# Performance work log

Measured on AMD Instinct MI355X. Metric: run time of the kernel, lower is better.

## Reference

```python
import jax, jax.numpy as jnp
import numpy as np

DIM = 768
HEADS = 12
HEAD_DIM = DIM // HEADS
SCALE = HEAD_DIM ** (-0.5)
BATCH = 1
SEQ = 4096


def setup_inputs() -> dict:
    key = jax.random.key(0)
    ks = jax.random.split(key, 5)
    x = jax.random.normal(ks[0], (BATCH, SEQ, DIM), dtype=jnp.float32)
    # Linear params stored (in, out) for y = x @ W + b
    w_qkv = jax.random.normal(ks[1], (DIM, 3 * DIM), dtype=jnp.float32) * (DIM ** -0.5)
    b_qkv = jnp.zeros((3 * DIM,), dtype=jnp.float32)
    w_proj = jax.random.normal(ks[2], (DIM, DIM), dtype=jnp.float32) * (DIM ** -0.5)
    b_proj = jnp.zeros((DIM,), dtype=jnp.float32)
    return {"x": x, "w_qkv": w_qkv, "b_qkv": b_qkv, "w_proj": w_proj, "b_proj": b_proj}


def reference(x, w_qkv, b_qkv, w_proj, b_proj):
    B, S, _ = x.shape
    qkv = x @ w_qkv + b_qkv                              # [B,S,3*DIM]
    qkv = qkv.reshape(B, S, 3, HEADS, HEAD_DIM)
    q, k, v = qkv[:, :, 0], qkv[:, :, 1], qkv[:, :, 2]   # [B,S,H,D]
    # scaled dot-product attention, full score matrix as in the original
    attn = jnp.einsum("bqhd,bkhd->bhqk", q * SCALE, k)   # [B,H,S,S]
    attn = jax.nn.softmax(attn, axis=-1)
    out = jnp.einsum("bhqk,bkhd->bqhd", attn, v)         # [B,S,H,D]
    out = out.reshape(B, S, DIM)
    return out @ w_proj + b_proj
```

## Files before the change

kernel.cpp:

```cpp
#include <hip/hip_runtime.h>
#include <hip/hip_bf16.h>

#define SEQ   4096
#define DIM   768
#define HEADS 12
#define NQKV  2304
#define QSCALE 0.18033688011f

#if __has_builtin(__builtin_amdgcn_exp2f)
#define EXP2(x) __builtin_amdgcn_exp2f(x)
#else
#define EXP2(x) __expf((x) * 0.69314718056f)
#endif

typedef __bf16 bf16_t;
typedef bf16_t bf16x8 __attribute__((ext_vector_type(8)));
typedef float  f32x4  __attribute__((ext_vector_type(4)));
typedef float  f32x16 __attribute__((ext_vector_type(16)));
typedef unsigned short u16;
typedef unsigned int   u32;

static __device__ __forceinline__ float bf2f(u16 v) {
    union { float f; unsigned u; } x; x.u = ((unsigned)v) << 16; return x.f;
}
static __device__ __forceinline__ u16 f2bf(float f) {
    union { float f; unsigned u; } x; x.f = f;
    unsigned r = x.u + 0x7fff + ((x.u >> 16) & 1);
    return (u16)(r >> 16);
}
static __device__ __forceinline__ u32 fbits(float f) {
    union { float f; unsigned u; } x; x.f = f; return x.u;
}
static __device__ __forceinline__ void gload_lds16(const u16* g, u16* l) {
    __builtin_amdgcn_global_load_lds(
        (const __attribute__((address_space(1))) unsigned int*)g,
        (__attribute__((address_space(3))) unsigned int*)l, 16, 0, 0);
}

static __device__ __forceinline__ int detect_f32(const u32* __restrict__ x) {
    int lane = threadIdx.x & 63;
    int cnt = 0;
#pragma unroll
    for (int i = 0; i < 8; ++i) {
        u32 w = x[lane * 8 + i];
        cnt += (((w >> 7) & 0xFF) >= 0x8F) ? 1 : 0;
    }
#pragma unroll
    for (int m = 1; m < 64; m <<= 1) cnt += __shfl_xor(cnt, m);
    return cnt >= 64;
}

__global__ __launch_bounds__(256) void prep(
    const void* __restrict__ x, const void* __restrict__ wqkv,
    const void* __restrict__ bqkv, const void* __restrict__ wproj,
    const void* __restrict__ bproj,
    u16* __restrict__ cvt, u16* __restrict__ wqkvT, u16* __restrict__ wprojT)
{
    __shared__ u16 tile[64][65];
    const bool f32 = detect_f32((const u32*)x) != 0;
    const int b = blockIdx.x;
    const int t = threadIdx.x;

    if (b < 576) {
        const void* src; u16* dst; int K, N, tx, ty;
        if (b < 432) { src = wqkv; dst = wqkvT; K = DIM; N = NQKV; tx = b % 36; ty = b / 36; }
        else { int bb = b - 432; src = wproj; dst = wprojT; K = DIM; N = DIM; tx = bb % 12; ty = bb / 12; }
        const int k0 = ty * 64, n0 = tx * 64;
#pragma unroll
        for (int i = 0; i < 16; ++i) {
            int idx = i * 256 + t;
            int r = idx >> 6, c = idx & 63;
            size_t si = (size_t)(k0 + r) * N + n0 + c;
            tile[r][c] = f32 ? f2bf(((const float*)src)[si]) : ((const u16*)src)[si];
        }
        __syncthreads();
#pragma unroll
        for (int i = 0; i < 16; ++i) {
            int idx = i * 256 + t;
            int r = idx >> 6, c = idx & 63;
            dst[(size_t)(n0 + r) * K + k0 + c] = tile[c][r];
        }
    } else {
        const int SX = SEQ * DIM, e1 = SX + NQKV;
        const int n_cvt = e1 + DIM;
        for (int i = (b - 576) * 256 + t; i < n_cvt; i += 200 * 256) {
            const void* s; int off;
            if      (i < SX) { s = x; off = i; }
            else if (i < e1) { s = bqkv; off = i - SX; }
            else             { s = bproj; off = i - e1; }
            cvt[i] = f32 ? f2bf(((const float*)s)[off]) : ((const u16*)s)[off];
        }
    }
}

template<int MODE>
__global__ __launch_bounds__(256) void gemm128(
    const u16* __restrict__ A, const u16* __restrict__ BT, const u16* __restrict__ bias,
    u16* __restrict__ C0, float* __restrict__ Cf, u16* __restrict__ VT,
    const u32* __restrict__ xdet, int M, int N, int K)
{
    __shared__ u16 a_lds[128 * 32];
    __shared__ u16 b_lds[128 * 32];

    const int t    = threadIdx.x;
    const int w    = t >> 6;
    const int lane = t & 63;
    const int l15  = lane & 15;
    const int quad = lane >> 4;
    const int wm   = w >> 1, wn = w & 1;
    const int m0   = blockIdx.y * 128, n0 = blockIdx.x * 128;

    const int srow = w * 32 + (lane >> 2);
    const int kch  = (lane & 3) * 8;
    const u16* asrc = A  + (size_t)(m0 + srow) * K + kch;
    const u16* bsrc = BT + (size_t)(n0 + srow) * K + kch;
    u16* adst = a_lds + w * 32 * 32;
    u16* bdst = b_lds + w * 32 * 32;

    f32x4 acc[4][4] = {};

    for (int kt = 0; kt < K; kt += 32) {
        __syncthreads();
        gload_lds16(asrc,          adst);
        gload_lds16(asrc + 16 * K, adst + 16 * 32);
        gload_lds16(bsrc,          bdst);
        gload_lds16(bsrc + 16 * K, bdst + 16 * 32);
        asrc += 32; bsrc += 32;
        __syncthreads();

        const u16* ab = a_lds + (wm * 64 + l15) * 32 + quad * 8;
        const u16* bb = b_lds + (wn * 64 + l15) * 32 + quad * 8;
        bf16x8 af[4], bfr[4];
#pragma unroll
        for (int i = 0; i < 4; ++i) af[i]  = *(const bf16x8*)(ab + i * 16 * 32);
#pragma unroll
        for (int j = 0; j < 4; ++j) bfr[j] = *(const bf16x8*)(bb + j * 16 * 32);
#pragma unroll
        for (int i = 0; i < 4; ++i)
#pragma unroll
            for (int j = 0; j < 4; ++j)
                acc[i][j] = __builtin_amdgcn_mfma_f32_16x16x32_bf16(af[i], bfr[j], acc[i][j], 0, 0, 0);
    }

    bool outf32 = false;
    if (MODE == 0) outf32 = detect_f32(xdet) != 0;
#pragma unroll
    for (int i = 0; i < 4; ++i)
#pragma unroll
        for (int j = 0; j < 4; ++j)
#pragma unroll
            for (int r = 0; r < 4; ++r) {
                int m = m0 + wm * 64 + i * 16 + quad * 4 + r;
                int n = n0 + wn * 64 + j * 16 + l15;
                float v = acc[i][j][r] + bf2f(bias[n]);
                if (MODE == 0) {
                    if (outf32) Cf[(size_t)m * N + n] = v;
                    else        C0[(size_t)m * N + n] = f2bf(v);
                } else {
                    if (n < 768) {
                        C0[(size_t)m * 1536 + n] = f2bf(v * QSCALE);
                    } else if (n < 1536) {
                        C0[(size_t)m * 1536 + n] = f2bf(v);
                    } else {
                        int mp = (m & ~15) | (m & 3) |
                                 (((m >> 2) & 1) << 3) | (((m >> 3) & 1) << 2);
                        VT[(size_t)(n - 1536) * SEQ + mp] = f2bf(v);
                    }
                }
            }
}

__global__ __launch_bounds__(256) void attn_kernel(
    const u16* __restrict__ qk, const u16* __restrict__ vt, u16* __restrict__ out)
{
    __shared__ u16 k_lds[3][64 * 64];
    __shared__ u16 v_lds[3][64 * 64];
    __shared__ float l_red[2][2][32];

    const int t    = threadIdx.x;
    const int w    = t >> 6;
    const int lane = t & 63;
    const int l31  = lane & 31;
    const int h    = lane >> 5;
    const int wq   = w & 1;
    const int wk   = w >> 1;

    const int lin     = blockIdx.x + (blockIdx.y << 6);
    const int logical = (lin & 7) * 96 + (lin >> 3);
    const int head    = logical >> 6;
    const int q0      = (logical & 63) * 64 + wq * 32;

    const u16* qrow = qk + (size_t)(q0 + l31) * 1536 + head * 64 + h * 8;
    bf16x8 qb[4];
#pragma unroll
    for (int s = 0; s < 4; ++s) qb[s] = *(const bf16x8*)(qrow + 16 * s);

    bf16x8 ones;
#pragma unroll
    for (int j = 0; j < 8; ++j) ones[j] = (bf16_t)1.0f;

    const int srow = 8 * w + (lane >> 3);
    const int cs   = ((lane & 7) - srow) & 7;
    const u16* kg = qk + 768 + head * 64 + (size_t)srow * 1536 + cs * 8;
    const u16* vg = vt + (size_t)head * 64 * SEQ + (size_t)srow * SEQ + cs * 8;
    const int woff = 8 * w * 64;

    const int krow = 32 * wk + l31;

    f32x16 o0 = {}, o1 = {}, lac = {};

    auto stage = [&](u16* kd, u16* vd, int T) {
        const u16* kgT = kg + (size_t)T * 64 * 1536;
        const u16* vgT = vg + (size_t)T * 64;
        gload_lds16(kgT,                      kd + woff);
        gload_lds16(kgT + (size_t)32 * 1536,  kd + woff + 32 * 64);
        gload_lds16(vgT,                      vd + woff);
        gload_lds16(vgT + (size_t)32 * SEQ,   vd + woff + 32 * 64);
    };

    auto compute = [&](const u16* kb, const u16* vb) {
        f32x16 st = {};
        __builtin_amdgcn_s_setprio(1);
#pragma unroll
        for (int s = 0; s < 4; ++s) {
            bf16x8 ka = *(const bf16x8*)(kb + krow * 64 + (((2 * s + h + krow) & 7) * 8));
            st = __builtin_amdgcn_mfma_f32_32x32x16_bf16(ka, qb[s], st, 0, 0, 0);
        }
        __builtin_amdgcn_s_setprio(0);
        u32 q32[8];
#pragma unroll
        for (int i = 0; i < 8; ++i) {
            float pe = EXP2(st[2 * i]);
            float po = EXP2(st[2 * i + 1]);
            q32[i] = __builtin_amdgcn_perm(fbits(po), fbits(pe), 0x07060302u);
        }
        union { u32 u[4]; bf16x8 v; } pf0, pf1;
#pragma unroll
        for (int i = 0; i < 4; ++i) { pf0.u[i] = q32[i]; pf1.u[i] = q32[4 + i]; }
        __builtin_amdgcn_s_setprio(1);
#pragma unroll
        for (int s2 = 0; s2 < 2; ++s2) {
            const int c = 4 * wk + 2 * s2 + h;
            bf16x8 vb0 = *(const bf16x8*)(vb + l31 * 64 + (((c + l31) & 7) * 8));
            bf16x8 vb1 = *(const bf16x8*)(vb + (32 + l31) * 64 + (((c + 32 + l31) & 7) * 8));
            const bf16x8 pv = s2 ? pf1.v : pf0.v;
            o0  = __builtin_amdgcn_mfma_f32_32x32x16_bf16(pv, vb0, o0, 0, 0, 0);
            o1  = __builtin_amdgcn_mfma_f32_32x32x16_bf16(pv, vb1, o1, 0, 0, 0);
            lac = __builtin_amdgcn_mfma_f32_32x32x16_bf16(pv, ones, lac, 0, 0, 0);
        }
        __builtin_amdgcn_s_setprio(0);
    };

    u16 *kA = &k_lds[0][0], *kB = &k_lds[1][0], *kC = &k_lds[2][0];
    u16 *vA = &v_lds[0][0], *vB = &v_lds[1][0], *vC = &v_lds[2][0];

    stage(kA, vA, 0);
    stage(kB, vB, 1);
    for (int T = 0; T < 62; ++T) {
        asm volatile("s_waitcnt vmcnt(4)" ::: "memory");
        __builtin_amdgcn_s_barrier();
        stage(kC, vC, T + 2);
        compute(kA, vA);
        u16* tk = kA; kA = kB; kB = kC; kC = tk;
        u16* tv = vA; vA = vB; vB = vC; vC = tv;
    }
    asm volatile("s_waitcnt vmcnt(4)" ::: "memory");
    __builtin_amdgcn_s_barrier();
    compute(kA, vA);
    asm volatile("s_waitcnt vmcnt(0)" ::: "memory");
    __builtin_amdgcn_s_barrier();
    compute(kB, vB);
    __syncthreads();

    if (l31 == 0) {
#pragma unroll
        for (int r = 0; r < 16; ++r) {
            int row = (r & 3) + 8 * (r >> 2) + 4 * h;
            l_red[wq][wk][row] = lac[r];
        }
    }
    float* scr = (wq == 0) ? (float*)&k_lds[0][0] : (float*)&v_lds[0][0];
    if (wk == 1) {
#pragma unroll
        for (int r = 0; r < 16; ++r) {
            int row = (r & 3) + 8 * (r >> 2) + 4 * h;
            scr[row * 64 + l31]      = o0[r];
            scr[row * 64 + 32 + l31] = o1[r];
        }
    }
    __syncthreads();
    if (wk == 0) {
#pragma unroll
        for (int r = 0; r < 16; ++r) {
            int row = (r & 3) + 8 * (r >> 2) + 4 * h;
            float lt   = l_red[wq][0][row] + l_red[wq][1][row];
            float invl = 1.0f / lt;
            float s0 = o0[r] + scr[row * 64 + l31];
            float s1 = o1[r] + scr[row * 64 + 32 + l31];
            size_t gr = (size_t)(q0 + row) * 768 + head * 64;
            out[gr + l31]      = f2bf(s0 * invl);
            out[gr + 32 + l31] = f2bf(s1 * invl);
        }
    }
}

extern "C" void kernel_launch(void* const* d_in, const int* in_sizes, int n_in,
                              void* d_out, int out_size, void* d_ws, size_t ws_size,
                              hipStream_t stream) {
    const int SX = SEQ * DIM;

    u16* base   = (u16*)d_ws;
    u16* xb     = base;
    u16* bqkvb  = xb + SX;
    u16* bprojb = bqkvb + NQKV;
    u16* wqkvT  = bprojb + DIM;
    u16* wprojT = wqkvT + (size_t)NQKV * DIM;
    u16* qkb    = wprojT + (size_t)DIM * DIM;
    u16* vtb    = qkb + (size_t)SEQ * 1536;
    u16* attnb  = xb;

    prep<<<776, 256, 0, stream>>>(
        d_in[0], d_in[1], d_in[2], d_in[3], d_in[4], base, wqkvT, wprojT);
    gemm128<1><<<dim3(NQKV / 128, SEQ / 128), 256, 0, stream>>>(
        xb, wqkvT, bqkvb, qkb, nullptr, vtb, (const u32*)d_in[0],
        SEQ, NQKV, DIM);
    attn_kernel<<<dim3(SEQ / 64, HEADS), 256, 0, stream>>>(qkb, vtb, attnb);
    gemm128<0><<<dim3(DIM / 128, SEQ / 128), 256, 0, stream>>>(
        attnb, wprojT, bprojb, (u16*)d_out, (float*)d_out, nullptr,
        (const u32*)d_in[0], SEQ, DIM, DIM);
}
```

Measured before the change: 232.4 us.

## Load V tiles directly into registers, drop the V LDS buffers

The attention loop no longer stages V tiles through a triple-buffered LDS area. Each wave loads its V fragments straight from global memory into registers, one tile ahead, using two register sets that alternate across a loop unrolled by two. K keeps its LDS triple buffer, and the wait counts are retuned to the new mix of loads. This removes the LDS writes and reads for V and halves shared memory use, which may allow more blocks per CU. The cost is more registers and V prefetched only one tile ahead, so global latency may be hidden less well.

Measured after the change: 292.7 us. 1.26x slower.

```diff
diff --git a/kernel.cpp b/kernel.cpp
--- a/kernel.cpp
+++ b/kernel.cpp
@@ -174,7 +174,6 @@
     const u16* __restrict__ qk, const u16* __restrict__ vt, u16* __restrict__ out)
 {
     __shared__ u16 k_lds[3][64 * 64];
-    __shared__ u16 v_lds[3][64 * 64];
     __shared__ float l_red[2][2][32];
 
     const int t    = threadIdx.x;
@@ -199,33 +198,46 @@
 #pragma unroll
     for (int j = 0; j < 8; ++j) ones[j] = (bf16_t)1.0f;
 
+    const f32x16 fz = {};
+
     const int srow = 8 * w + (lane >> 3);
     const int cs   = ((lane & 7) - srow) & 7;
-    const u16* kg = qk + 768 + head * 64 + (size_t)srow * 1536 + cs * 8;
-    const u16* vg = vt + (size_t)head * 64 * SEQ + (size_t)srow * SEQ + cs * 8;
+    const u16* kst0 = qk + 768 + head * 64 + (size_t)srow * 1536 + cs * 8;
+    const u16* kst1 = kst0 + (size_t)32 * 1536;
     const int woff = 8 * w * 64;
 
+    const u16* vp0 = vt + ((size_t)head * 64 + l31) * SEQ + (4 * wk + h) * 8;
+    const u16* vp1 = vp0 + (size_t)32 * SEQ;
+
     const int krow = 32 * wk + l31;
 
     f32x16 o0 = {}, o1 = {}, lac = {};
 
-    auto stage = [&](u16* kd, u16* vd, int T) {
-        const u16* kgT = kg + (size_t)T * 64 * 1536;
-        const u16* vgT = vg + (size_t)T * 64;
-        gload_lds16(kgT,                      kd + woff);
-        gload_lds16(kgT + (size_t)32 * 1536,  kd + woff + 32 * 64);
-        gload_lds16(vgT,                      vd + woff);
-        gload_lds16(vgT + (size_t)32 * SEQ,   vd + woff + 32 * 64);
+    auto STAGEK = [&](u16* kd) {
+        gload_lds16(kst0, kd + woff);
+        gload_lds16(kst1, kd + woff + 32 * 64);
+        kst0 += (size_t)64 * 1536;
+        kst1 += (size_t)64 * 1536;
     };
-
-    auto compute = [&](const u16* kb, const u16* vb) {
-        f32x16 st = {};
+    auto VPRE = [&](bf16x8& d0, bf16x8& d1, bf16x8& d2, bf16x8& d3) {
+        d0 = *(const bf16x8*)(vp0);
+        d1 = *(const bf16x8*)(vp0 + 16);
+        d2 = *(const bf16x8*)(vp1);
+        d3 = *(const bf16x8*)(vp1 + 16);
+        vp0 += 64; vp1 += 64;
+    };
+
+    auto compute = [&](const u16* kb, bf16x8 v00, bf16x8 v01, bf16x8 v10, bf16x8 v11) {
+        const u16* kbase = kb + krow * 64;
+        bf16x8 ka0 = *(const bf16x8*)(kbase + (((0 + h + krow) & 7) * 8));
+        bf16x8 ka1 = *(const bf16x8*)(kbase + (((2 + h + krow) & 7) * 8));
+        bf16x8 ka2 = *(const bf16x8*)(kbase + (((4 + h + krow) & 7) * 8));
+        bf16x8 ka3 = *(const bf16x8*)(kbase + (((6 + h + krow) & 7) * 8));
         __builtin_amdgcn_s_setprio(1);
-#pragma unroll
-        for (int s = 0; s < 4; ++s) {
-            bf16x8 ka = *(const bf16x8*)(kb + krow * 64 + (((2 * s + h + krow) & 7) * 8));
-            st = __builtin_amdgcn_mfma_f32_32x32x16_bf16(ka, qb[s], st, 0, 0, 0);
-        }
+        f32x16 st = __builtin_amdgcn_mfma_f32_32x32x16_bf16(ka0, qb[0], fz, 0, 0, 0);
+        st = __builtin_amdgcn_mfma_f32_32x32x16_bf16(ka1, qb[1], st, 0, 0, 0);
+        st = __builtin_amdgcn_mfma_f32_32x32x16_bf16(ka2, qb[2], st, 0, 0, 0);
+        st = __builtin_amdgcn_mfma_f32_32x32x16_bf16(ka3, qb[3], st, 0, 0, 0);
         __builtin_amdgcn_s_setprio(0);
         u32 q32[8];
 #pragma unroll
@@ -238,38 +250,43 @@
 #pragma unroll
         for (int i = 0; i < 4; ++i) { pf0.u[i] = q32[i]; pf1.u[i] = q32[4 + i]; }
         __builtin_amdgcn_s_setprio(1);
-#pragma unroll
-        for (int s2 = 0; s2 < 2; ++s2) {
-            const int c = 4 * wk + 2 * s2 + h;
-            bf16x8 vb0 = *(const bf16x8*)(vb + l31 * 64 + (((c + l31) & 7) * 8));
-            bf16x8 vb1 = *(const bf16x8*)(vb + (32 + l31) * 64 + (((c + 32 + l31) & 7) * 8));
-            const bf16x8 pv = s2 ? pf1.v : pf0.v;
-            o0  = __builtin_amdgcn_mfma_f32_32x32x16_bf16(pv, vb0, o0, 0, 0, 0);
-            o1  = __builtin_amdgcn_mfma_f32_32x32x16_bf16(pv, vb1, o1, 0, 0, 0);
-            lac = __builtin_amdgcn_mfma_f32_32x32x16_bf16(pv, ones, lac, 0, 0, 0);
-        }
+        o0  = __builtin_amdgcn_mfma_f32_32x32x16_bf16(pf0.v, v00, o0, 0, 0, 0);
+        o1  = __builtin_amdgcn_mfma_f32_32x32x16_bf16(pf0.v, v10, o1, 0, 0, 0);
+        lac = __builtin_amdgcn_mfma_f32_32x32x16_bf16(pf0.v, ones, lac, 0, 0, 0);
+        o0  = __builtin_amdgcn_mfma_f32_32x32x16_bf16(pf1.v, v01, o0, 0, 0, 0);
+        o1  = __builtin_amdgcn_mfma_f32_32x32x16_bf16(pf1.v, v11, o1, 0, 0, 0);
+        lac = __builtin_amdgcn_mfma_f32_32x32x16_bf16(pf1.v, ones, lac, 0, 0, 0);
         __builtin_amdgcn_s_setprio(0);
     };
 
+    bf16x8 a0, a1, a2, a3, b0, b1, b2, b3;
     u16 *kA = &k_lds[0][0], *kB = &k_lds[1][0], *kC = &k_lds[2][0];
-    u16 *vA = &v_lds[0][0], *vB = &v_lds[1][0], *vC = &v_lds[2][0];
-
-    stage(kA, vA, 0);
-    stage(kB, vB, 1);
-    for (int T = 0; T < 62; ++T) {
-        asm volatile("s_waitcnt vmcnt(4)" ::: "memory");
+
+    VPRE(a0, a1, a2, a3);
+    STAGEK(kA);
+    STAGEK(kB);
+    for (int T = 0; T < 62; T += 2) {
+        asm volatile("s_waitcnt vmcnt(2)" ::: "memory");
         __builtin_amdgcn_s_barrier();
-        stage(kC, vC, T + 2);
-        compute(kA, vA);
-        u16* tk = kA; kA = kB; kB = kC; kC = tk;
-        u16* tv = vA; vA = vB; vB = vC; vC = tv;
-    }
-    asm volatile("s_waitcnt vmcnt(4)" ::: "memory");
+        VPRE(b0, b1, b2, b3);
+        STAGEK(kC);
+        compute(kA, a0, a1, a2, a3);
+        { u16* tt = kA; kA = kB; kB = kC; kC = tt; }
+        asm volatile("s_waitcnt vmcnt(2)" ::: "memory");
+        __builtin_amdgcn_s_barrier();
+        VPRE(a0, a1, a2, a3);
+        STAGEK(kC);
+        compute(kA, b0, b1, b2, b3);
+        { u16* tt = kA; kA = kB; kB = kC; kC = tt; }
+    }
+    asm volatile("s_waitcnt vmcnt(2)" ::: "memory");
     __builtin_amdgcn_s_barrier();
-    compute(kA, vA);
+    VPRE(b0, b1, b2, b3);
+    compute(kA, a0, a1, a2, a3);
+    { u16* tt = kA; kA = kB; kB = kC; kC = tt; }
     asm volatile("s_waitcnt vmcnt(0)" ::: "memory");
     __builtin_amdgcn_s_barrier();
-    compute(kB, vB);
+    compute(kA, b0, b1, b2, b3);
     __syncthreads();
 
     if (l31 == 0) {
@@ -279,7 +296,7 @@
             l_red[wq][wk][row] = lac[r];
         }
     }
-    float* scr = (wq == 0) ? (float*)&k_lds[0][0] : (float*)&v_lds[0][0];
+    float* scr = (wq == 0) ? (float*)&k_lds[0][0] : (float*)&k_lds[1][0];
     if (wk == 1) {
 #pragma unroll
         for (int r = 0; r < 16; ++r) {
```

## Software-pipeline QK of next tile with softmax-PV of current tile in attention

Applied to the files above, without the earlier changes.

Restructures the attention main loop so the QK^T MFMAs for tile T+1 are issued before the exp/PV work for tile T, splitting K and V staging into separate loads with pointer increments. The loop is manually unrolled by two to rotate score registers. This aims to overlap the exp (transcendental) work with matrix-core work and separate K/V load timing. It also adds a launch_bounds occupancy hint of 3 blocks per CU, which may constrain registers while an extra score accumulator is now live.

New measurement: 221.7 us. 4.6% less time.

```diff
diff --git a/kernel.cpp b/kernel.cpp
--- a/kernel.cpp
+++ b/kernel.cpp
@@ -170,7 +170,7 @@
             }
 }
 
-__global__ __launch_bounds__(256) void attn_kernel(
+__global__ __launch_bounds__(256, 3) void attn_kernel(
     const u16* __restrict__ qk, const u16* __restrict__ vt, u16* __restrict__ out)
 {
     __shared__ u16 k_lds[3][64 * 64];
@@ -199,34 +199,49 @@
 #pragma unroll
     for (int j = 0; j < 8; ++j) ones[j] = (bf16_t)1.0f;
 
+    const f32x16 fz = {};
+
     const int srow = 8 * w + (lane >> 3);
     const int cs   = ((lane & 7) - srow) & 7;
-    const u16* kg = qk + 768 + head * 64 + (size_t)srow * 1536 + cs * 8;
-    const u16* vg = vt + (size_t)head * 64 * SEQ + (size_t)srow * SEQ + cs * 8;
+    const u16* kst0 = qk + 768 + head * 64 + (size_t)srow * 1536 + cs * 8;
+    const u16* kst1 = kst0 + (size_t)32 * 1536;
+    const u16* vst0 = vt + (size_t)head * 64 * SEQ + (size_t)srow * SEQ + cs * 8;
+    const u16* vst1 = vst0 + (size_t)32 * SEQ;
     const int woff = 8 * w * 64;
 
     const int krow = 32 * wk + l31;
 
     f32x16 o0 = {}, o1 = {}, lac = {};
 
-    auto stage = [&](u16* kd, u16* vd, int T) {
-        const u16* kgT = kg + (size_t)T * 64 * 1536;
-        const u16* vgT = vg + (size_t)T * 64;
-        gload_lds16(kgT,                      kd + woff);
-        gload_lds16(kgT + (size_t)32 * 1536,  kd + woff + 32 * 64);
-        gload_lds16(vgT,                      vd + woff);
-        gload_lds16(vgT + (size_t)32 * SEQ,   vd + woff + 32 * 64);
+    auto SK = [&](u16* kd) {
+        gload_lds16(kst0, kd + woff);
+        gload_lds16(kst1, kd + woff + 32 * 64);
+        kst0 += (size_t)64 * 1536;
+        kst1 += (size_t)64 * 1536;
     };
-
-    auto compute = [&](const u16* kb, const u16* vb) {
-        f32x16 st = {};
+    auto SV = [&](u16* vd) {
+        gload_lds16(vst0, vd + woff);
+        gload_lds16(vst1, vd + woff + 32 * 64);
+        vst0 += 64;
+        vst1 += 64;
+    };
+
+    auto QK = [&](const u16* kb) -> f32x16 {
+        const u16* kbase = kb + krow * 64;
+        bf16x8 ka0 = *(const bf16x8*)(kbase + (((0 + h + krow) & 7) * 8));
+        bf16x8 ka1 = *(const bf16x8*)(kbase + (((2 + h + krow) & 7) * 8));
+        bf16x8 ka2 = *(const bf16x8*)(kbase + (((4 + h + krow) & 7) * 8));
+        bf16x8 ka3 = *(const bf16x8*)(kbase + (((6 + h + krow) & 7) * 8));
         __builtin_amdgcn_s_setprio(1);
-#pragma unroll
-        for (int s = 0; s < 4; ++s) {
-            bf16x8 ka = *(const bf16x8*)(kb + krow * 64 + (((2 * s + h + krow) & 7) * 8));
-            st = __builtin_amdgcn_mfma_f32_32x32x16_bf16(ka, qb[s], st, 0, 0, 0);
-        }
+        f32x16 st = __builtin_amdgcn_mfma_f32_32x32x16_bf16(ka0, qb[0], fz, 0, 0, 0);
+        st = __builtin_amdgcn_mfma_f32_32x32x16_bf16(ka1, qb[1], st, 0, 0, 0);
+        st = __builtin_amdgcn_mfma_f32_32x32x16_bf16(ka2, qb[2], st, 0, 0, 0);
+        st = __builtin_amdgcn_mfma_f32_32x32x16_bf16(ka3, qb[3], st, 0, 0, 0);
         __builtin_amdgcn_s_setprio(0);
+        return st;
+    };
+
+    auto SMPV = [&](const f32x16& st, const u16* vb) {
         u32 q32[8];
 #pragma unroll
         for (int i = 0; i < 8; ++i) {
@@ -254,22 +269,42 @@
     u16 *kA = &k_lds[0][0], *kB = &k_lds[1][0], *kC = &k_lds[2][0];
     u16 *vA = &v_lds[0][0], *vB = &v_lds[1][0], *vC = &v_lds[2][0];
 
-    stage(kA, vA, 0);
-    stage(kB, vB, 1);
-    for (int T = 0; T < 62; ++T) {
+    SK(kA);
+    SV(vA);
+    SK(kB);
+    asm volatile("s_waitcnt vmcnt(4)" ::: "memory");
+    __builtin_amdgcn_s_barrier();
+    f32x16 stA = QK(kA);
+    SV(vB);
+    f32x16 stB;
+
+    for (int i = 0; i < 31; ++i) {
+        SK(kC);
         asm volatile("s_waitcnt vmcnt(4)" ::: "memory");
         __builtin_amdgcn_s_barrier();
-        stage(kC, vC, T + 2);
-        compute(kA, vA);
-        u16* tk = kA; kA = kB; kB = kC; kC = tk;
-        u16* tv = vA; vA = vB; vB = vC; vC = tv;
-    }
-    asm volatile("s_waitcnt vmcnt(4)" ::: "memory");
+        stB = QK(kB);
+        SMPV(stA, vA);
+        SV(vC);
+        { u16* tt = kA; kA = kB; kB = kC; kC = tt; }
+        { u16* tt = vA; vA = vB; vB = vC; vC = tt; }
+        SK(kC);
+        asm volatile("s_waitcnt vmcnt(4)" ::: "memory");
+        __builtin_amdgcn_s_barrier();
+        stA = QK(kB);
+        SMPV(stB, vA);
+        SV(vC);
+        { u16* tt = kA; kA = kB; kB = kC; kC = tt; }
+        { u16* tt = vA; vA = vB; vB = vC; vC = tt; }
+    }
+    asm volatile("s_waitcnt vmcnt(2)" ::: "memory");
     __builtin_amdgcn_s_barrier();
-    compute(kA, vA);
+    stB = QK(kB);
+    SMPV(stA, vA);
+    { u16* tt = kA; kA = kB; kB = kC; kC = tt; }
+    { u16* tt = vA; vA = vB; vB = vC; vC = tt; }
     asm volatile("s_waitcnt vmcnt(0)" ::: "memory");
     __builtin_amdgcn_s_barrier();
-    compute(kB, vB);
+    SMPV(stB, vA);
     __syncthreads();
 
     if (l31 == 0) {
```
